# Performance work log

Hardware: AMD Instinct MI355X
Metric: run time of the kernel (lower is better)

The kernel has to match this reference:

```python
import jax, jax.numpy as jnp
import numpy as np

N = 20000          # graph_size
IN_DIM = 256
H, D = 3, 64       # num_heads (hardcoded 3 in source), out_dim
E = 640000         # N * avg_degree(32)
NEG_SLOPE = 0.2    # DGL GATConv default negative_slope


def setup_inputs() -> dict:
    key = jax.random.key(0)
    ks = jax.random.split(key, 8)
    feat = jax.random.normal(ks[0], (N, IN_DIM), dtype=jnp.float32)
    W = jax.random.normal(ks[1], (IN_DIM, H * D), dtype=jnp.float32) * 0.05
    attn_l = jax.random.normal(ks[2], (H, D), dtype=jnp.float32) * 0.05
    attn_r = jax.random.normal(ks[3], (H, D), dtype=jnp.float32) * 0.05
    gat_bias = jnp.zeros((H * D,), dtype=jnp.float32)
    fc_w = jax.random.normal(ks[4], (N * H * D, 2), dtype=jnp.float32) * 0.001
    fc_b = jnp.zeros((2,), dtype=jnp.float32)
    src = jax.random.randint(ks[5], (E,), 0, N, dtype=jnp.int64)
    dst = jax.random.randint(ks[6], (E,), 0, N, dtype=jnp.int64)
    return {"feat": feat, "W": W, "attn_l": attn_l, "attn_r": attn_r,
            "gat_bias": gat_bias, "fc_w": fc_w, "fc_b": fc_b,
            "src": src, "dst": dst}


def reference(feat, W, attn_l, attn_r, gat_bias, fc_w, fc_b, src, dst):
    n = feat.shape[0]
    # GATConv: projected multi-head features [N, H, D]
    h = (feat @ W).reshape(n, H, D)
    el = jnp.einsum('nhd,hd->nh', h, attn_l)   # [N, H]
    er = jnp.einsum('nhd,hd->nh', h, attn_r)   # [N, H]
    # per-edge raw attention logits, LeakyReLU(el[src] + er[dst])
    e = jax.nn.leaky_relu(el[src] + er[dst], negative_slope=NEG_SLOPE)  # [E, H]
    # edge-softmax grouped by destination node (stable)
    m = jax.ops.segment_max(e, dst, num_segments=n)   # [N, H]
    ex = jnp.exp(e - m[dst])
    denom = jax.ops.segment_sum(ex, dst, num_segments=n)  # [N, H]
    alpha = ex / denom[dst]                            # [E, H]
    # weighted message aggregation: out[v] = sum_{(u->v)} alpha * h[u]
    msg = h[src] * alpha[:, :, None]                   # [E, H, D]
    out = jax.ops.segment_sum(msg, dst, num_segments=n)  # [N, H, D]
    out = out + gat_bias.reshape(H, D)                 # GATConv bias
    out = jax.nn.relu(out)                             # self.activation
    # Flatten(start_dim=0) -> Linear(N*H*D, 2)
    return out.reshape(-1) @ fc_w + fc_b               # [2]
```

## Files before the change

### kernel.cpp

```cpp
#include <hip/hip_runtime.h>
#include <hip/hip_bf16.h>
#include <cstdint>
#include <cstddef>

#define INDIM  256
#define HD     192
#define NHEADS 3
#define NEG_SLOPE 0.2f
#define ELLPAD 96
#define LPAD   97
#define BSHIFT 6
#define BNODES 64
#define NBUCKP 320
#define BCAP   2432
#define P1CHUNK 4096

typedef __attribute__((ext_vector_type(8))) short short8;
typedef __attribute__((ext_vector_type(4))) float f32x4;

__device__ __forceinline__ float wave_sum(float v) {
#pragma unroll
    for (int o = 32; o; o >>= 1) v += __shfl_xor(v, o, 64);
    return v;
}

__global__ __launch_bounds__(256) void prep_kernel(
    const float* __restrict__ W, __hip_bfloat16* __restrict__ Wt,
    int* __restrict__ gCur)
{
    const int b = blockIdx.x, tid = threadIdx.x;
    if (b == 0) {
        for (int i = tid; i < NBUCKP; i += 256) gCur[i] = 0;
        return;
    }
    int n = b - 1;
    Wt[n * 256 + tid] = __float2bfloat16(W[tid * HD + n]);
}

__global__ __launch_bounds__(256) void gemm_bucket_kernel(
    const float* __restrict__ feat,
    const __hip_bfloat16* __restrict__ Wt,
    const float* __restrict__ attn_l, const float* __restrict__ attn_r,
    __hip_bfloat16* __restrict__ hb, float* __restrict__ el,
    float* __restrict__ er, int M,
    const int* __restrict__ src, const int* __restrict__ dst,
    int* __restrict__ gCur, int2* __restrict__ pairs,
    int E, int gemmBlocks)
{
    const int tid = threadIdx.x;
    if (blockIdx.x >= gemmBlocks) {
        __shared__ int cnt[NBUCKP];
        __shared__ int cnt2[NBUCKP];
        __shared__ int base[NBUCKP];
        const int e0 = (blockIdx.x - gemmBlocks) * P1CHUNK;
        for (int i = tid; i < NBUCKP; i += 256) { cnt[i] = 0; cnt2[i] = 0; }
        __syncthreads();
#pragma unroll
        for (int u = 0; u < 16; u++) {
            int e = e0 + u * 256 + tid;
            if (e < E) atomicAdd(&cnt[dst[e] >> BSHIFT], 1);
        }
        __syncthreads();
        for (int i = tid; i < NBUCKP; i += 256)
            if (cnt[i] > 0) base[i] = atomicAdd(&gCur[i], cnt[i]);
        __syncthreads();
#pragma unroll
        for (int u = 0; u < 16; u++) {
            int e = e0 + u * 256 + tid;
            if (e < E) {
                int d = dst[e];
                int b = d >> BSHIFT;
                int l = atomicAdd(&cnt2[b], 1);
                int idx = base[b] + l;
                if (idx < BCAP)
                    pairs[(size_t)b * BCAP + idx] = make_int2(d, src[e]);
            }
        }
        return;
    }
    __shared__ __hip_bfloat16 As[64][40];
    __shared__ __hip_bfloat16 Bs[192][40];
    const int lane = tid & 63, w = tid >> 6;
    const int q = lane >> 4, ll = lane & 15;
    const int row0 = blockIdx.x * 64;

    f32x4 acc[12];
#pragma unroll
    for (int c = 0; c < 12; c++) acc[c] = (f32x4){0.f, 0.f, 0.f, 0.f};

    const int sr = tid >> 2, sk = (tid & 3) * 8;

    for (int k0 = 0; k0 < INDIM; k0 += 32) {
        __syncthreads();
        float4 a0 = make_float4(0.f, 0.f, 0.f, 0.f), a1 = a0;
        int grow = row0 + sr;
        if (grow < M) {
            const float* ap = feat + (size_t)grow * INDIM + k0 + sk;
            a0 = *(const float4*)ap;
            a1 = *(const float4*)(ap + 4);
        }
        __hip_bfloat16 ab[8] = {__float2bfloat16(a0.x), __float2bfloat16(a0.y),
                                __float2bfloat16(a0.z), __float2bfloat16(a0.w),
                                __float2bfloat16(a1.x), __float2bfloat16(a1.y),
                                __float2bfloat16(a1.z), __float2bfloat16(a1.w)};
        *(uint4*)&As[sr][sk] = *(const uint4*)ab;
        if (tid < HD) {
            const __hip_bfloat16* bp = Wt + (size_t)tid * INDIM + k0;
            uint4 b0 = *(const uint4*)bp;
            uint4 b1 = *(const uint4*)(bp + 8);
            uint4 b2 = *(const uint4*)(bp + 16);
            uint4 b3 = *(const uint4*)(bp + 24);
            *(uint4*)&Bs[tid][0]  = b0;
            *(uint4*)&Bs[tid][8]  = b1;
            *(uint4*)&Bs[tid][16] = b2;
            *(uint4*)&Bs[tid][24] = b3;
        }
        __syncthreads();

        short8 af = *(const short8*)&As[w * 16 + ll][q * 8];
#pragma unroll
        for (int c = 0; c < 12; c++) {
            short8 bf = *(const short8*)&Bs[c * 16 + ll][q * 8];
            acc[c] = __builtin_amdgcn_mfma_f32_16x16x32_bf16(af, bf, acc[c], 0, 0, 0);
        }
    }

    float al[12], ar[12];
#pragma unroll
    for (int c = 0; c < 12; c++) {
        al[c] = attn_l[c * 16 + ll];
        ar[c] = attn_r[c * 16 + ll];
    }
    float sl[3][4], sr_[3][4];
#pragma unroll
    for (int hd = 0; hd < 3; hd++)
#pragma unroll
        for (int i = 0; i < 4; i++) {
            float a = 0.f, b = 0.f;
#pragma unroll
            for (int f = 0; f < 4; f++) {
                a = fmaf(acc[hd * 4 + f][i], al[hd * 4 + f], a);
                b = fmaf(acc[hd * 4 + f][i], ar[hd * 4 + f], b);
            }
            sl[hd][i] = a; sr_[hd][i] = b;
        }
#pragma unroll
    for (int hd = 0; hd < 3; hd++)
#pragma unroll
        for (int i = 0; i < 4; i++)
#pragma unroll
            for (int off = 1; off < 16; off <<= 1) {
                sl[hd][i]  += __shfl_xor(sl[hd][i],  off, 64);
                sr_[hd][i] += __shfl_xor(sr_[hd][i], off, 64);
            }
#pragma unroll
    for (int c = 0; c < 12; c++)
#pragma unroll
        for (int i = 0; i < 4; i++) {
            int row = row0 + w * 16 + q * 4 + i;
            if (row < M)
                hb[(size_t)row * HD + c * 16 + ll] = __float2bfloat16(acc[c][i]);
        }
    if (ll == 0) {
#pragma unroll
        for (int i = 0; i < 4; i++) {
            int row = row0 + w * 16 + q * 4 + i;
            if (row < M) {
#pragma unroll
                for (int hd = 0; hd < 3; hd++) {
                    el[row * 4 + hd] = sl[hd][i];
                    er[row * 4 + hd] = sr_[hd][i];
                }
            }
        }
    }
}

__global__ __launch_bounds__(1024) void gat_bucket_kernel(
    const __hip_bfloat16* __restrict__ h, const float* __restrict__ el,
    const float* __restrict__ er, const int2* __restrict__ pairs,
    const int* __restrict__ gCur, const float* __restrict__ gbias,
    const float* __restrict__ fc_w, float* __restrict__ pA,
    float* __restrict__ pB, int N)
{
    __shared__ int cur[BNODES];
    __shared__ int lell[BNODES][LPAD];
    __shared__ float4 sE[16][64];

    const int b = blockIdx.x;
    const int tid = threadIdx.x;
    const int lane = tid & 63, wslot = tid >> 6;

    if (tid < BNODES) cur[tid] = 0;
    __syncthreads();
    const int pcnt = min(gCur[b], BCAP);
    const int2* pp = pairs + (size_t)b * BCAP;
    for (int i = tid; i < pcnt; i += 1024) {
        int2 p = pp[i];
        int nl = p.x & (BNODES - 1);
        int r = atomicAdd(&cur[nl], 1);
        if (r < ELLPAD) lell[nl][r] = p.y;
    }
    __syncthreads();

    const __hip_bfloat16* hl = h + lane;

#pragma unroll 1
    for (int k = 0; k < 4; k++) {
        const int nl = (wslot << 2) + k;
        const int v = (b << BSHIFT) + nl;
        if (v >= N) continue;

        const int cnt = min(cur[nl], ELLPAD);
        const int* rowp = &lell[nl][0];
        const float4 erv = ((const float4*)er)[v];
        const float er0 = erv.x, er1 = erv.y, er2 = erv.z;

        float acc0 = 0.f, acc1 = 0.f, acc2 = 0.f;
        float d0 = 0.f, d1 = 0.f, d2 = 0.f;

        for (int chunk = 0; chunk < cnt; chunk += 64) {
            const int i = chunk + lane;
            float w0 = 0.f, w1 = 0.f, w2 = 0.f;
            int s = 0;
            if (i < cnt) {
                s = rowp[i];
                const float4 le = ((const float4*)el)[s];
                float l0 = le.x + er0;
                float l1 = le.y + er1;
                float l2 = le.z + er2;
                l0 = l0 > 0.f ? l0 : NEG_SLOPE * l0;
                l1 = l1 > 0.f ? l1 : NEG_SLOPE * l1;
                l2 = l2 > 0.f ? l2 : NEG_SLOPE * l2;
                w0 = __expf(l0); w1 = __expf(l1); w2 = __expf(l2);
            }
            d0 += w0; d1 += w1; d2 += w2;
            sE[wslot][lane] = make_float4(__int_as_float(s), w0, w1, w2);
            __asm__ volatile("s_waitcnt lgkmcnt(0)" ::: "memory");

            const int rem = min(cnt - chunk, 64);
            const int nR = (rem + 7) & ~7;
            for (int j = 0; j < nR; j += 8) {
                float4 e[8];
#pragma unroll
                for (int u = 0; u < 8; u++) e[u] = sE[wslot][j + u];
                float x0[8], x1[8], x2[8];
#pragma unroll
                for (int u = 0; u < 8; u++) {
                    const __hip_bfloat16* p = hl + (size_t)__float_as_int(e[u].x) * HD;
                    x0[u] = __bfloat162float(p[0]);
                    x1[u] = __bfloat162float(p[64]);
                    x2[u] = __bfloat162float(p[128]);
                }
#pragma unroll
                for (int u = 0; u < 8; u++) {
                    acc0 = fmaf(e[u].y, x0[u], acc0);
                    acc1 = fmaf(e[u].z, x1[u], acc1);
                    acc2 = fmaf(e[u].w, x2[u], acc2);
                }
            }
        }

        d0 = wave_sum(d0); d1 = wave_sum(d1); d2 = wave_sum(d2);

        float o0 = (d0 > 0.f) ? acc0 / d0 : 0.f;
        float o1 = (d1 > 0.f) ? acc1 / d1 : 0.f;
        float o2 = (d2 > 0.f) ? acc2 / d2 : 0.f;
        o0 = fmaxf(o0 + gbias[lane], 0.f);
        o1 = fmaxf(o1 + gbias[64 + lane], 0.f);
        o2 = fmaxf(o2 + gbias[128 + lane], 0.f);

        const size_t bidx = (size_t)v * HD;
        float2 w0v = ((const float2*)fc_w)[bidx + lane];
        float2 w1v = ((const float2*)fc_w)[bidx + 64 + lane];
        float2 w2v = ((const float2*)fc_w)[bidx + 128 + lane];
        float f0 = fmaf(o0, w0v.x, fmaf(o1, w1v.x, o2 * w2v.x));
        float f1 = fmaf(o0, w0v.y, fmaf(o1, w1v.y, o2 * w2v.y));

        f0 = wave_sum(f0); f1 = wave_sum(f1);
        if (lane == 0) { pA[v] = f0; pB[v] = f1; }
    }
}

__global__ __launch_bounds__(1024) void final_reduce(const float* __restrict__ pA,
                                                     const float* __restrict__ pB,
                                                     const float* __restrict__ fc_b,
                                                     float* __restrict__ out, int nb)
{
    int tid = threadIdx.x;
    float s0 = 0.f, s1 = 0.f;
    for (int i = tid; i < nb; i += 1024) { s0 += pA[i]; s1 += pB[i]; }
    s0 = wave_sum(s0); s1 = wave_sum(s1);
    __shared__ float sh[32];
    int lane = tid & 63, w = tid >> 6;
    if (lane == 0) { sh[w * 2] = s0; sh[w * 2 + 1] = s1; }
    __syncthreads();
    if (tid == 0) {
        float t0 = 0.f, t1 = 0.f;
#pragma unroll
        for (int i = 0; i < 16; i++) { t0 += sh[i * 2]; t1 += sh[i * 2 + 1]; }
        out[0] = t0 + fc_b[0];
        out[1] = t1 + fc_b[1];
    }
}

extern "C" void kernel_launch(void* const* d_in, const int* in_sizes, int n_in,
                              void* d_out, int out_size, void* d_ws, size_t ws_size,
                              hipStream_t stream)
{
    const float* feat   = (const float*)d_in[0];
    const float* W      = (const float*)d_in[1];
    const float* attn_l = (const float*)d_in[2];
    const float* attn_r = (const float*)d_in[3];
    const float* gbias  = (const float*)d_in[4];
    const float* fc_w   = (const float*)d_in[5];
    const float* fc_b   = (const float*)d_in[6];
    const int*   src    = (const int*)d_in[7];
    const int*   dst    = (const int*)d_in[8];

    const int N = in_sizes[0] / INDIM;
    const int E = in_sizes[7];
    const int nBuck = (N + BNODES - 1) >> BSHIFT;

    __hip_bfloat16* Wt = (__hip_bfloat16*)d_ws;
    __hip_bfloat16* hb = Wt + HD * INDIM;
    float* el = (float*)(hb + (size_t)N * HD);
    float* er = el + (size_t)N * 4;
    int* gCur = (int*)(er + (size_t)N * 4);
    int2* pairs = (int2*)(gCur + NBUCKP);
    float* pA = (float*)(pairs + (size_t)NBUCKP * BCAP);
    float* pB = pA + N;

    prep_kernel<<<1 + HD, 256, 0, stream>>>(W, Wt, gCur);

    const int gemmBlocks = (N + 63) / 64;
    const int p1Blocks = (E + P1CHUNK - 1) / P1CHUNK;
    gemm_bucket_kernel<<<gemmBlocks + p1Blocks, 256, 0, stream>>>(
        feat, Wt, attn_l, attn_r, hb, el, er, N,
        src, dst, gCur, pairs, E, gemmBlocks);

    gat_bucket_kernel<<<nBuck, 1024, 0, stream>>>(hb, el, er, pairs, gCur,
                                                  gbias, fc_w, pA, pB, N);
    final_reduce<<<1, 1024, 0, stream>>>(pA, pB, fc_b, (float*)d_out, N);
}
```

Baseline: 169.8 us.

## Shrink destination buckets to 16 nodes and register-prefetch GEMM tiles

After: 177.0 us. 1.04x slower.

```diff
diff --git a/kernel.cpp b/kernel.cpp
--- a/kernel.cpp
+++ b/kernel.cpp
@@ -9,11 +9,11 @@
 #define NEG_SLOPE 0.2f
 #define ELLPAD 96
 #define LPAD   97
-#define BSHIFT 6
-#define BNODES 64
-#define NBUCKP 320
-#define BCAP   2432
-#define P1CHUNK 4096
+#define BSHIFT 4
+#define BNODES 16
+#define NBUCKP 1280
+#define BCAP   704
+#define P1CHUNK 8192
 
 typedef __attribute__((ext_vector_type(8))) short short8;
 typedef __attribute__((ext_vector_type(4))) float f32x4;
@@ -55,8 +55,7 @@
         const int e0 = (blockIdx.x - gemmBlocks) * P1CHUNK;
         for (int i = tid; i < NBUCKP; i += 256) { cnt[i] = 0; cnt2[i] = 0; }
         __syncthreads();
-#pragma unroll
-        for (int u = 0; u < 16; u++) {
+        for (int u = 0; u < P1CHUNK / 256; u++) {
             int e = e0 + u * 256 + tid;
             if (e < E) atomicAdd(&cnt[dst[e] >> BSHIFT], 1);
         }
@@ -64,8 +63,7 @@
         for (int i = tid; i < NBUCKP; i += 256)
             if (cnt[i] > 0) base[i] = atomicAdd(&gCur[i], cnt[i]);
         __syncthreads();
-#pragma unroll
-        for (int u = 0; u < 16; u++) {
+        for (int u = 0; u < P1CHUNK / 256; u++) {
             int e = e0 + u * 256 + tid;
             if (e < E) {
                 int d = dst[e];
@@ -89,32 +87,43 @@
     for (int c = 0; c < 12; c++) acc[c] = (f32x4){0.f, 0.f, 0.f, 0.f};
 
     const int sr = tid >> 2, sk = (tid & 3) * 8;
+    const int grow = row0 + sr;
+    const bool arow = grow < M;
+    const float* ap = feat + (size_t)grow * INDIM + sk;
+    const __hip_bfloat16* bp = Wt + (size_t)tid * INDIM;
+
+    float4 a0 = make_float4(0.f, 0.f, 0.f, 0.f), a1 = a0;
+    if (arow) { a0 = *(const float4*)ap; a1 = *(const float4*)(ap + 4); }
+    uint4 b0, b1, b2, b3;
+    if (tid < HD) {
+        b0 = *(const uint4*)(bp);      b1 = *(const uint4*)(bp + 8);
+        b2 = *(const uint4*)(bp + 16); b3 = *(const uint4*)(bp + 24);
+    }
 
     for (int k0 = 0; k0 < INDIM; k0 += 32) {
-        __syncthreads();
-        float4 a0 = make_float4(0.f, 0.f, 0.f, 0.f), a1 = a0;
-        int grow = row0 + sr;
-        if (grow < M) {
-            const float* ap = feat + (size_t)grow * INDIM + k0 + sk;
-            a0 = *(const float4*)ap;
-            a1 = *(const float4*)(ap + 4);
-        }
         __hip_bfloat16 ab[8] = {__float2bfloat16(a0.x), __float2bfloat16(a0.y),
                                 __float2bfloat16(a0.z), __float2bfloat16(a0.w),
                                 __float2bfloat16(a1.x), __float2bfloat16(a1.y),
                                 __float2bfloat16(a1.z), __float2bfloat16(a1.w)};
+        __syncthreads();
         *(uint4*)&As[sr][sk] = *(const uint4*)ab;
         if (tid < HD) {
-            const __hip_bfloat16* bp = Wt + (size_t)tid * INDIM + k0;
-            uint4 b0 = *(const uint4*)bp;
-            uint4 b1 = *(const uint4*)(bp + 8);
-            uint4 b2 = *(const uint4*)(bp + 16);
-            uint4 b3 = *(const uint4*)(bp + 24);
             *(uint4*)&Bs[tid][0]  = b0;
             *(uint4*)&Bs[tid][8]  = b1;
             *(uint4*)&Bs[tid][16] = b2;
             *(uint4*)&Bs[tid][24] = b3;
         }
+        if (k0 + 32 < INDIM) {
+            if (arow) {
+                a0 = *(const float4*)(ap + k0 + 32);
+                a1 = *(const float4*)(ap + k0 + 36);
+            }
+            if (tid < HD) {
+                const __hip_bfloat16* bq = bp + k0 + 32;
+                b0 = *(const uint4*)(bq);      b1 = *(const uint4*)(bq + 8);
+                b2 = *(const uint4*)(bq + 16); b3 = *(const uint4*)(bq + 24);
+            }
+        }
         __syncthreads();
 
         short8 af = *(const short8*)&As[w * 16 + ll][q * 8];
@@ -176,7 +185,7 @@
     }
 }
 
-__global__ __launch_bounds__(1024) void gat_bucket_kernel(
+__global__ __launch_bounds__(256) void gat_bucket_kernel(
     const __hip_bfloat16* __restrict__ h, const float* __restrict__ el,
     const float* __restrict__ er, const int2* __restrict__ pairs,
     const int* __restrict__ gCur, const float* __restrict__ gbias,
@@ -185,7 +194,7 @@
 {
     __shared__ int cur[BNODES];
     __shared__ int lell[BNODES][LPAD];
-    __shared__ float4 sE[16][64];
+    __shared__ float4 sE[4][64];
 
     const int b = blockIdx.x;
     const int tid = threadIdx.x;
@@ -195,7 +204,7 @@
     __syncthreads();
     const int pcnt = min(gCur[b], BCAP);
     const int2* pp = pairs + (size_t)b * BCAP;
-    for (int i = tid; i < pcnt; i += 1024) {
+    for (int i = tid; i < pcnt; i += 256) {
         int2 p = pp[i];
         int nl = p.x & (BNODES - 1);
         int r = atomicAdd(&cur[nl], 1);
@@ -339,7 +348,7 @@
         feat, Wt, attn_l, attn_r, hb, el, er, N,
         src, dst, gCur, pairs, E, gemmBlocks);
 
-    gat_bucket_kernel<<<nBuck, 1024, 0, stream>>>(hb, el, er, pairs, gCur,
-                                                  gbias, fc_w, pA, pB, N);
+    gat_bucket_kernel<<<nBuck, 256, 0, stream>>>(hb, el, er, pairs, gCur,
+                                                 gbias, fc_w, pA, pB, N);
     final_reduce<<<1, 1024, 0, stream>>>(pA, pB, fc_b, (float*)d_out, N);
 }
```
